# Optimization experiments

Measured on AMD Instinct MI355X. Metric: run time of the kernel, lower is better.

Reference implementation:

```python
import jax, jax.numpy as jnp
import numpy as np

B, S, D = 2, 2048, 512
H, HD = 8, 64  # num_heads, hidden_dim; H*HD == D
FF = 2048
EPS = 1e-5


def layer_norm(x, gamma, beta):
    mu = jnp.mean(x, axis=-1, keepdims=True)
    var = jnp.mean(jnp.square(x - mu), axis=-1, keepdims=True)
    return (x - mu) * jax.lax.rsqrt(var + EPS) * gamma + beta


def setup_inputs() -> dict:
    key = jax.random.key(0)
    ks = jax.random.split(key, 16)
    s = 0.02
    return {
        "Q": jax.random.normal(ks[0], (B, S, D), jnp.float32),
        "K": jax.random.normal(ks[1], (B, S, D), jnp.float32),
        "V": jax.random.normal(ks[2], (B, S, D), jnp.float32),
        "mask": jax.random.randint(ks[3], (B, S, S), 0, 2, jnp.int32),
        "Wq": jax.random.normal(ks[4], (D, H * HD), jnp.float32) * s,
        "Wk": jax.random.normal(ks[5], (D, H * HD), jnp.float32) * s,
        "Wv": jax.random.normal(ks[6], (D, H * HD), jnp.float32) * s,
        "Wo": jax.random.normal(ks[7], (H * HD, D), jnp.float32) * s,
        "bo": jnp.zeros((D,), jnp.float32),
        "gamma": jnp.ones((D,), jnp.float32),
        "beta": jnp.zeros((D,), jnp.float32),
        "W1": jax.random.normal(ks[8], (D, FF), jnp.float32) * s,
        "b1": jnp.zeros((FF,), jnp.float32),
        "W2": jax.random.normal(ks[9], (FF, D), jnp.float32) * s,
        "b2": jnp.zeros((D,), jnp.float32),
    }


def reference(Q, K, V, mask, Wq, Wk, Wv, Wo, bo, gamma, beta, W1, b1, W2, b2):
    # NOTE: original torch code calls Z.masked_fill(...) non-inplace and drops
    # the result, so `mask` has no effect on the math. Sequence=False.
    X = V
    # Faithful (interleaving) reshape: [B, S, H*HD] -> [B*H, S, HD]
    q = (Q @ Wq).reshape(B * H, -1, HD)
    k = (K @ Wk).reshape(B * H, -1, HD)
    v = (V @ Wv).reshape(B * H, -1, HD)
    scale = jnp.sqrt(jnp.float32(D))  # sqrt(input_size[2]), not sqrt(hidden_dim)
    scores = jnp.einsum('bqd,bkd->bqk', q, k) / scale  # [B*H, S, S]
    attn = jax.nn.softmax(scores, axis=2)
    Z = jnp.einsum('bqk,bkd->bqd', attn, v)            # [B*H, S, HD]
    Z = Z.reshape(B, -1, H * HD) @ Wo + bo             # [B, S, D]
    Z = layer_norm(X + Z, gamma, beta)
    ffn = (Z @ W1 + b1) @ W2 + b2                      # no activation in source
    return layer_norm(Z + ffn, gamma, beta)
```

## Files before the change

### kernel.cpp

```cpp
#include <hip/hip_runtime.h>
#include <hip/hip_bf16.h>


typedef __hip_bfloat16 bf16;
typedef short s16x8 __attribute__((ext_vector_type(8)));
typedef short s16x4 __attribute__((ext_vector_type(4)));
typedef float f32x4 __attribute__((ext_vector_type(4)));

#if __has_builtin(__builtin_amdgcn_exp2f)
#define EXP2F(x) __builtin_amdgcn_exp2f(x)
#else
#define EXP2F(x) exp2f(x)
#endif

__device__ __forceinline__ int dtypeF32(const void* gamma) {
    return *(const unsigned int*)gamma == 0x3F800000u;
}
__device__ __forceinline__ float inElem(const void* p, size_t i, int f32) {
    return f32 ? ((const float*)p)[i]
               : __bfloat162float(((const bf16*)p)[i]);
}
__device__ __forceinline__ void outElem(void* p, size_t i, float v, int f32) {
    if (f32) ((float*)p)[i] = v;
    else     ((bf16*)p)[i] = __float2bfloat16(v);
}
__device__ __forceinline__ s16x8 load8bf(const void* p, size_t i, int f32) {
    if (f32) {
        const float* s = (const float*)p + i;
        const float4 a = *(const float4*)s;
        const float4 b = *(const float4*)(s + 4);
        bf16 t[8] = {__float2bfloat16(a.x), __float2bfloat16(a.y),
                     __float2bfloat16(a.z), __float2bfloat16(a.w),
                     __float2bfloat16(b.x), __float2bfloat16(b.y),
                     __float2bfloat16(b.z), __float2bfloat16(b.w)};
        return *(const s16x8*)t;
    }
    return *(const s16x8*)((const bf16*)p + i);
}

__global__ __launch_bounds__(256) void tr_kernel(const void* __restrict__ s0,
                                                 const void* __restrict__ s1,
                                                 const void* __restrict__ s2,
                                                 const void* __restrict__ s3,
                                                 const void* __restrict__ s4,
                                                 bf16* __restrict__ WT4,
                                                 bf16* __restrict__ W2T,
                                                 float scale0,
                                                 const void* __restrict__ gamma) {
    const int z = blockIdx.z;
    if (z < 4 && blockIdx.y >= 16) return;
    const int f32 = dtypeF32(gamma);
    const void* src = z == 0 ? s0 : (z == 1 ? s1 : (z == 2 ? s2 : (z == 3 ? s3 : s4)));
    const int R = (z == 4) ? 2048 : 512;
    const int C = 512;
    bf16* d = (z == 4) ? W2T : WT4 + (size_t)z * 512 * 512;
    const float sc = (z == 0) ? scale0 : 1.f;
    __shared__ bf16 T[32][33];
    const int tx = threadIdx.x & 31, ty = threadIdx.x >> 5;
    const int c0 = blockIdx.x * 32, r0 = blockIdx.y * 32;
#pragma unroll
    for (int i = 0; i < 4; ++i)
        T[ty + 8 * i][tx] = __float2bfloat16(
            sc * inElem(src, (size_t)(r0 + ty + 8 * i) * C + c0 + tx, f32));
    __syncthreads();
#pragma unroll
    for (int i = 0; i < 4; ++i)
        d[(size_t)(c0 + ty + 8 * i) * R + r0 + tx] = T[tx][ty + 8 * i];
}

__global__ __launch_bounds__(64) void bc_kernel(const bf16* __restrict__ W2T,
                                                const void* __restrict__ b1,
                                                const void* __restrict__ b2,
                                                const void* __restrict__ bo,
                                                float* __restrict__ bc,
                                                float* __restrict__ bo_f,
                                                const void* __restrict__ gamma) {
    const int f32 = dtypeF32(gamma);
    const int n = blockIdx.x, lane = threadIdx.x;
    const bf16* row = W2T + (size_t)n * 2048;
    float s = 0.f;
#pragma unroll
    for (int i = 0; i < 32; ++i) {
        const int f = lane + 64 * i;
        s += inElem(b1, f, f32) * __bfloat162float(row[f]);
    }
#pragma unroll
    for (int off = 32; off; off >>= 1) s += __shfl_xor(s, off);
    if (lane == 0) {
        bc[n] = s + inElem(b2, n, f32);
        bo_f[n] = inElem(bo, n, f32);
    }
}

__global__ __launch_bounds__(256) void gemm_ks_kernel(
    const bf16* __restrict__ A, const void* __restrict__ Bt,
    float* __restrict__ Cf, const void* __restrict__ gamma) {
    __shared__ __align__(16) unsigned short As[64][40];
    __shared__ __align__(16) unsigned short Bs[128][40];

    const int bF = dtypeF32(gamma);
    const int N = 512, K = 2048, kSlice = 512;
    const int tid = threadIdx.x;
    const int w = tid >> 6, lane = tid & 63, quad = lane >> 4, l16 = lane & 15;
    const int wr = w >> 1, wc = w & 1;
    const int row0 = blockIdx.y * 64, col0 = blockIdx.x * 128;
    const int sr = tid >> 2, sc = (tid & 3) * 8;
    const int kOff = blockIdx.z * kSlice;
    float* C = Cf + (size_t)blockIdx.z * N * N;

    f32x4 acc[2][4];
#pragma unroll
    for (int rb = 0; rb < 2; ++rb)
#pragma unroll
        for (int nb = 0; nb < 4; ++nb) acc[rb][nb] = (f32x4){0.f, 0.f, 0.f, 0.f};

    for (int k0 = kOff; k0 < kOff + kSlice; k0 += 32) {
        __syncthreads();
        *(s16x8*)&As[sr][sc] = *(const s16x8*)(A + (size_t)(row0 + sr) * K + k0 + sc);
        *(s16x8*)&Bs[sr][sc] = load8bf(Bt, (size_t)(col0 + sr) * K + k0 + sc, bF);
        *(s16x8*)&Bs[sr + 64][sc] = load8bf(Bt, (size_t)(col0 + sr + 64) * K + k0 + sc, bF);
        __syncthreads();

        s16x8 aF[2], bFr[4];
#pragma unroll
        for (int rb = 0; rb < 2; ++rb)
            aF[rb] = *(const s16x8*)&As[wr * 32 + rb * 16 + l16][quad * 8];
#pragma unroll
        for (int nb = 0; nb < 4; ++nb)
            bFr[nb] = *(const s16x8*)&Bs[wc * 64 + nb * 16 + l16][quad * 8];
#pragma unroll
        for (int rb = 0; rb < 2; ++rb)
#pragma unroll
            for (int nb = 0; nb < 4; ++nb)
                acc[rb][nb] = __builtin_amdgcn_mfma_f32_16x16x32_bf16(
                    aF[rb], bFr[nb], acc[rb][nb], 0, 0, 0);
    }

#pragma unroll
    for (int rb = 0; rb < 2; ++rb)
#pragma unroll
        for (int nb = 0; nb < 4; ++nb) {
            const int col = col0 + wc * 64 + nb * 16 + l16;
#pragma unroll
            for (int r = 0; r < 4; ++r) {
                const int row = row0 + wr * 32 + rb * 16 + quad * 4 + r;
                C[(size_t)row * N + col] = acc[rb][nb][r];
            }
        }
}

__global__ __launch_bounds__(256) void combine4_kernel(const float* __restrict__ Cf,
                                                       bf16* __restrict__ WcT) {
    const int i0 = (blockIdx.x * 256 + threadIdx.x) * 4;
    const int MN = 512 * 512;
#pragma unroll
    for (int j = 0; j < 4; ++j) {
        const int i = i0 + j;
        WcT[i] = __float2bfloat16(Cf[i] + Cf[i + MN] + Cf[i + 2 * MN] + Cf[i + 3 * MN]);
    }
}

__global__ __launch_bounds__(256) void gemm_qkv_kernel(
    const void* __restrict__ Q, const void* __restrict__ K,
    const void* __restrict__ V,
    const bf16* __restrict__ WT4, bf16* __restrict__ Cbase,
    const void* __restrict__ gamma) {
    __shared__ __align__(16) unsigned short As[64][40];
    __shared__ __align__(16) unsigned short Bs[256][40];

    const int aF = dtypeF32(gamma);
    const int z = blockIdx.z;
    const void* A = z == 0 ? Q : (z == 1 ? K : V);
    const bf16* Bt = WT4 + (size_t)z * 512 * 512;
    bf16* C = Cbase + (size_t)z * 4096 * 512;

    const int tid = threadIdx.x;
    const int w = tid >> 6, lane = tid & 63, quad = lane >> 4, l16 = lane & 15;
    const int wr = w >> 1, wc = w & 1;
    const int row0 = blockIdx.y * 64, col0 = blockIdx.x * 256;
    const int sr = tid >> 2, sc = (tid & 3) * 8;

    f32x4 acc[2][8];
#pragma unroll
    for (int rb = 0; rb < 2; ++rb)
#pragma unroll
        for (int nb = 0; nb < 8; ++nb) acc[rb][nb] = (f32x4){0.f, 0.f, 0.f, 0.f};

    for (int k0 = 0; k0 < 512; k0 += 32) {
        __syncthreads();
        *(s16x8*)&As[sr][sc] = load8bf(A, (size_t)(row0 + sr) * 512 + k0 + sc, aF);
#pragma unroll
        for (int i = 0; i < 4; ++i) {
            const int br = sr + 64 * i;
            *(s16x8*)&Bs[br][sc] = *(const s16x8*)(Bt + (size_t)(col0 + br) * 512 + k0 + sc);
        }
        __syncthreads();

        s16x8 aFr[2];
#pragma unroll
        for (int rb = 0; rb < 2; ++rb)
            aFr[rb] = *(const s16x8*)&As[wr * 32 + rb * 16 + l16][quad * 8];
#pragma unroll
        for (int nb = 0; nb < 8; ++nb) {
            const s16x8 bFr = *(const s16x8*)&Bs[wc * 128 + nb * 16 + l16][quad * 8];
#pragma unroll
            for (int rb = 0; rb < 2; ++rb)
                acc[rb][nb] = __builtin_amdgcn_mfma_f32_16x16x32_bf16(
                    aFr[rb], bFr, acc[rb][nb], 0, 0, 0);
        }
    }

#pragma unroll
    for (int rb = 0; rb < 2; ++rb)
#pragma unroll
        for (int nb = 0; nb < 8; ++nb) {
            const int col = col0 + wc * 128 + nb * 16 + l16;
#pragma unroll
            for (int r = 0; r < 4; ++r) {
                const int row = row0 + wr * 32 + rb * 16 + quad * 4 + r;
                C[(size_t)row * 512 + col] = __float2bfloat16(acc[rb][nb][r]);
            }
        }
}

__global__ __launch_bounds__(256) void pack_kernel(const bf16* __restrict__ Kp,
                                                   const bf16* __restrict__ Vp,
                                                   bf16* __restrict__ KF,
                                                   bf16* __restrict__ VF) {
    const int b = blockIdx.x;
    if (b < 1024) {
        const int fid = b * 256 + threadIdx.x;
        const int lane = fid & 63, l16 = lane & 15, quad = lane >> 4;
        const int ks = (fid >> 6) & 1;
        const int jb = (fid >> 7) & 127;
        const int g = fid >> 14;
        const bf16* src = Kp + ((size_t)g * 2048 + jb * 16 + l16) * 64 + ks * 32 + quad * 8;
        *(s16x8*)(KF + (size_t)fid * 8) = *(const s16x8*)src;
    } else {
        const int fid = (b - 1024) * 256 + threadIdx.x;
        const int lane = fid & 63, l16 = lane & 15, quad = lane >> 4;
        const int db = (fid >> 6) & 3;
        const int jb = (fid >> 8) & 127;
        const int g = fid >> 15;
        bf16 t[4];
#pragma unroll
        for (int r = 0; r < 4; ++r)
            t[r] = Vp[((size_t)g * 2048 + jb * 16 + quad * 4 + r) * 64 + db * 16 + l16];
        *(s16x4*)(VF + (size_t)fid * 4) = *(const s16x4*)t;
    }
}

__global__ __launch_bounds__(256) void attn_mfma_kernel(const bf16* __restrict__ Qp,
                                                        const bf16* __restrict__ KF,
                                                        const bf16* __restrict__ VF,
                                                        bf16* __restrict__ Z) {
    const int SG = 2048;
    __shared__ __align__(16) unsigned short KsF[2][4096];
    __shared__ __align__(16) unsigned short VsF[2][4096];

    const int tid = threadIdx.x;
    const int w = tid >> 6;
    const int lane = tid & 63;
    const int quad = lane >> 4;
    const int l16 = lane & 15;

    const int g = blockIdx.x & 15;
    const int qt = blockIdx.x >> 4;
    const int qrow = g * SG + qt * 64 + w * 16 + l16;

    s16x8 bQ[2];
#pragma unroll
    for (int ks = 0; ks < 2; ++ks)
        bQ[ks] = *(const s16x8*)(Qp + (size_t)qrow * 64 + ks * 32 + quad * 8);

    f32x4 o[4];
#pragma unroll
    for (int db = 0; db < 4; ++db) o[db] = (f32x4){0.f, 0.f, 0.f, 0.f};
    f32x4 oSum = (f32x4){0.f, 0.f, 0.f, 0.f};
    const s16x4 aOnes = {(short)0x3F80, (short)0x3F80, (short)0x3F80, (short)0x3F80};

    const bf16* KFg = KF + (size_t)g * 131072;
    const bf16* VFg = VF + (size_t)g * 131072;

    s16x8 pk[2], pv[2];
#pragma unroll
    for (int i = 0; i < 2; ++i) {
        const int idx = tid + 256 * i;
        pk[i] = *(const s16x8*)(KFg + (size_t)idx * 8);
        pv[i] = *(const s16x8*)(VFg + (size_t)idx * 8);
    }
#pragma unroll
    for (int i = 0; i < 2; ++i) {
        const int idx = tid + 256 * i;
        *(s16x8*)&KsF[0][idx * 8] = pk[i];
        *(s16x8*)&VsF[0][idx * 8] = pv[i];
    }
    __syncthreads();

    for (int t = 0; t < 32; ++t) {
        const int cur = t & 1, nxt = cur ^ 1;
        if (t + 1 < 32) {
            const bf16* kt = KFg + (size_t)(t + 1) * 4096;
            const bf16* vt = VFg + (size_t)(t + 1) * 4096;
#pragma unroll
            for (int i = 0; i < 2; ++i) {
                const int idx = tid + 256 * i;
                pk[i] = *(const s16x8*)(kt + (size_t)idx * 8);
                pv[i] = *(const s16x8*)(vt + (size_t)idx * 8);
            }
        }

        f32x4 st[4];
#pragma unroll
        for (int kb = 0; kb < 4; ++kb) st[kb] = (f32x4){0.f, 0.f, 0.f, 0.f};
#pragma unroll
        for (int kb = 0; kb < 4; ++kb)
#pragma unroll
            for (int ks = 0; ks < 2; ++ks) {
                const s16x8 aK = *(const s16x8*)&KsF[cur][((kb * 2 + ks) * 64 + lane) * 8];
                st[kb] = __builtin_amdgcn_mfma_f32_16x16x32_bf16(aK, bQ[ks], st[kb], 0, 0, 0);
            }

        s16x4 bP[4];
#pragma unroll
        for (int kb = 0; kb < 4; ++kb) {
            const float p0 = EXP2F(st[kb][0]);
            const float p1 = EXP2F(st[kb][1]);
            const float p2 = EXP2F(st[kb][2]);
            const float p3 = EXP2F(st[kb][3]);
            const unsigned lo = __builtin_amdgcn_perm(
                __builtin_bit_cast(unsigned, p1), __builtin_bit_cast(unsigned, p0), 0x07060302u);
            const unsigned hi = __builtin_amdgcn_perm(
                __builtin_bit_cast(unsigned, p3), __builtin_bit_cast(unsigned, p2), 0x07060302u);
            union { unsigned u[2]; s16x4 v; } cvt;
            cvt.u[0] = lo; cvt.u[1] = hi;
            bP[kb] = cvt.v;
        }

#pragma unroll
        for (int kb = 0; kb < 4; ++kb) {
            oSum = __builtin_amdgcn_mfma_f32_16x16x16bf16_1k(aOnes, bP[kb], oSum, 0, 0, 0);
#pragma unroll
            for (int db = 0; db < 4; ++db) {
                const s16x4 aV = *(const s16x4*)&VsF[cur][((kb * 4 + db) * 64 + lane) * 4];
                o[db] = __builtin_amdgcn_mfma_f32_16x16x16bf16_1k(aV, bP[kb], o[db], 0, 0, 0);
            }
        }

        if (t + 1 < 32) {
            __syncthreads();
#pragma unroll
            for (int i = 0; i < 2; ++i) {
                const int idx = tid + 256 * i;
                *(s16x8*)&KsF[nxt][idx * 8] = pk[i];
                *(s16x8*)&VsF[nxt][idx * 8] = pv[i];
            }
            __syncthreads();
        }
    }

    const float inv = 1.f / oSum[0];
#pragma unroll
    for (int db = 0; db < 4; ++db) {
        bf16 tmp[4];
#pragma unroll
        for (int r = 0; r < 4; ++r) tmp[r] = __float2bfloat16(o[db][r] * inv);
        *(s16x4*)(Z + (size_t)qrow * 64 + db * 16 + quad * 4) = *(const s16x4*)tmp;
    }
}

__global__ __launch_bounds__(256) void gemm_bt_kernel(
    const bf16* __restrict__ A, const bf16* __restrict__ Bt,
    const float* __restrict__ bias, bf16* __restrict__ C,
    int M, int N, int K) {
    __shared__ __align__(16) unsigned short As[64][40];
    __shared__ __align__(16) unsigned short Bs[128][40];

    const int tid = threadIdx.x;
    const int w = tid >> 6, lane = tid & 63, quad = lane >> 4, l16 = lane & 15;
    const int wr = w >> 1, wc = w & 1;
    const int row0 = blockIdx.y * 64, col0 = blockIdx.x * 128;
    const int sr = tid >> 2, sc = (tid & 3) * 8;

    f32x4 acc[2][4];
#pragma unroll
    for (int rb = 0; rb < 2; ++rb)
#pragma unroll
        for (int nb = 0; nb < 4; ++nb) acc[rb][nb] = (f32x4){0.f, 0.f, 0.f, 0.f};

    for (int k0 = 0; k0 < K; k0 += 32) {
        __syncthreads();
        *(s16x8*)&As[sr][sc] = *(const s16x8*)(A + (size_t)(row0 + sr) * K + k0 + sc);
        *(s16x8*)&Bs[sr][sc] = *(const s16x8*)(Bt + (size_t)(col0 + sr) * K + k0 + sc);
        *(s16x8*)&Bs[sr + 64][sc] = *(const s16x8*)(Bt + (size_t)(col0 + sr + 64) * K + k0 + sc);
        __syncthreads();

        s16x8 aF[2], bF[4];
#pragma unroll
        for (int rb = 0; rb < 2; ++rb)
            aF[rb] = *(const s16x8*)&As[wr * 32 + rb * 16 + l16][quad * 8];
#pragma unroll
        for (int nb = 0; nb < 4; ++nb)
            bF[nb] = *(const s16x8*)&Bs[wc * 64 + nb * 16 + l16][quad * 8];
#pragma unroll
        for (int rb = 0; rb < 2; ++rb)
#pragma unroll
            for (int nb = 0; nb < 4; ++nb)
                acc[rb][nb] = __builtin_amdgcn_mfma_f32_16x16x32_bf16(
                    aF[rb], bF[nb], acc[rb][nb], 0, 0, 0);
    }

#pragma unroll
    for (int rb = 0; rb < 2; ++rb)
#pragma unroll
        for (int nb = 0; nb < 4; ++nb) {
            const int col = col0 + wc * 64 + nb * 16 + l16;
            const float bv = bias[col];
#pragma unroll
            for (int r = 0; r < 4; ++r) {
                const int row = row0 + wr * 32 + rb * 16 + quad * 4 + r;
                C[(size_t)row * N + col] = __float2bfloat16(acc[rb][nb][r] + bv);
            }
        }
}

__global__ __launch_bounds__(256) void ln_res_kernel(const void* __restrict__ X, int xMode,
                                                     const bf16* __restrict__ Zin,
                                                     const void* __restrict__ gamma,
                                                     const void* __restrict__ beta,
                                                     void* __restrict__ out, int oMode) {
    const int f = dtypeF32(gamma);
    const int xF = xMode == 2 ? f : xMode;
    const int oF = oMode == 2 ? f : oMode;
    const int row = blockIdx.x * 4 + (threadIdx.x >> 6);
    const int lane = threadIdx.x & 63;
    const size_t rb = (size_t)row * 512;

    float v[8];
    float sum = 0.f, sumsq = 0.f;
#pragma unroll
    for (int i = 0; i < 8; ++i) {
        const int c = lane + 64 * i;
        const float x = inElem(X, rb + c, xF) + __bfloat162float(Zin[rb + c]);
        v[i] = x;
        sum += x;
        sumsq += x * x;
    }
#pragma unroll
    for (int off = 32; off; off >>= 1) {
        sum += __shfl_xor(sum, off);
        sumsq += __shfl_xor(sumsq, off);
    }
    const float mu = sum * (1.f / 512.f);
    const float var = sumsq * (1.f / 512.f) - mu * mu;
    const float rs = rsqrtf(var + 1e-5f);
#pragma unroll
    for (int i = 0; i < 8; ++i) {
        const int c = lane + 64 * i;
        const float gm = inElem(gamma, c, f);
        const float bt = inElem(beta, c, f);
        outElem(out, rb + c, (v[i] - mu) * rs * gm + bt, oF);
    }
}

extern "C" void kernel_launch(void* const* d_in, const int* in_sizes, int n_in,
                              void* d_out, int out_size, void* d_ws, size_t ws_size,
                              hipStream_t stream) {
    const void* Q     = d_in[0];
    const void* K     = d_in[1];
    const void* V     = d_in[2];
    const void* Wq    = d_in[4];
    const void* Wk    = d_in[5];
    const void* Wv    = d_in[6];
    const void* Wo    = d_in[7];
    const void* bo    = d_in[8];
    const void* gamma = d_in[9];
    const void* beta  = d_in[10];
    const void* W1    = d_in[11];
    const void* b1    = d_in[12];
    const void* W2    = d_in[13];
    const void* b2    = d_in[14];

    const int M = 4096;
    const size_t NT  = (size_t)M * 512;
    const size_t WSQ = 512 * 512;
    const size_t W1N = 512 * 2048;

    const size_t NEED = 27000000;
    char* scratch = (ws_size >= NEED) ? (char*)d_ws : (char*)d_in[3];

    bf16* base = (bf16*)scratch;
    bf16* Qp  = base;
    bf16* Kp  = Qp + NT;
    bf16* Vp  = Kp + NT;
    bf16* KF  = Vp + NT;
    bf16* VF  = KF + NT;
    bf16* WT4 = VF + NT;
    bf16* W2T = WT4 + 4 * WSQ;
    bf16* WcT = W2T + W1N;
    float* bc   = (float*)(WcT + WSQ);
    float* bo_f = bc + 512;
    float* Wc32 = (float*)VF;
    bf16* Zt = Kp;
    bf16* Zo = Qp;
    bf16* Z1 = Vp;
    bf16* Fo = KF;

    const dim3 blk(256);
    const float qscale = 1.4426950408889634f * 0.044194173824159216f;

    tr_kernel<<<dim3(16, 64, 5), blk, 0, stream>>>(Wq, Wk, Wv, Wo, W2,
                                                   WT4, W2T, qscale, gamma);
    bc_kernel<<<dim3(512), dim3(64), 0, stream>>>(W2T, b1, b2, bo, bc, bo_f, gamma);

    gemm_ks_kernel<<<dim3(4, 8, 4), blk, 0, stream>>>(W2T, W1, Wc32, gamma);
    combine4_kernel<<<dim3(256), blk, 0, stream>>>(Wc32, WcT);

    gemm_qkv_kernel<<<dim3(2, 64, 3), blk, 0, stream>>>(Q, K, V, WT4, Qp, gamma);

    pack_kernel<<<dim3(3072), blk, 0, stream>>>(Kp, Vp, KF, VF);

    attn_mfma_kernel<<<dim3(512), blk, 0, stream>>>(Qp, KF, VF, Zt);

    gemm_bt_kernel<<<dim3(4, 64), blk, 0, stream>>>(Zt, WT4 + 3 * WSQ, bo_f,
                                                    Zo, M, 512, 512);
    ln_res_kernel<<<dim3(1024), blk, 0, stream>>>(V, 2, Zo, gamma, beta, Z1, 0);

    gemm_bt_kernel<<<dim3(4, 64), blk, 0, stream>>>(Z1, WcT, bc, Fo, M, 512, 512);
    ln_res_kernel<<<dim3(1024), blk, 0, stream>>>(Z1, 0, Fo, gamma, beta, d_out, 2);
}
```

Baseline: 237.8 us.

## Use direct global-to-LDS loads and larger KV tiles in attention kernel

The attention kernel now copies K/V tiles from global memory straight into LDS with global_load_lds, so the data no longer passes through registers. It also doubles the tile to 128 keys, halving the loop trips and leaving one barrier per iteration instead of two. The intent is to cut register pressure, barrier overhead and load latency. The cost is twice the LDS (64KB per block), which may lower occupancy. Correctness also depends on global_load_lds completing before the single barrier without an explicit vmcnt wait.

```diff
diff --git a/kernel.cpp b/kernel.cpp
--- a/kernel.cpp
+++ b/kernel.cpp
@@ -36,6 +36,13 @@
         return *(const s16x8*)t;
     }
     return *(const s16x8*)((const bf16*)p + i);
+}
+
+__device__ __forceinline__ void gll16(const bf16* g, unsigned short* l) {
+    __builtin_amdgcn_global_load_lds(
+        (const __attribute__((address_space(1))) unsigned int*)(const void*)g,
+        (__attribute__((address_space(3))) unsigned int*)(void*)l,
+        16, 0, 0);
 }
 
 __global__ __launch_bounds__(256) void tr_kernel(const void* __restrict__ s0,
@@ -255,8 +262,8 @@
                                                         const bf16* __restrict__ VF,
                                                         bf16* __restrict__ Z) {
     const int SG = 2048;
-    __shared__ __align__(16) unsigned short KsF[2][4096];
-    __shared__ __align__(16) unsigned short VsF[2][4096];
+    __shared__ __align__(16) unsigned short KsF[2][8192];
+    __shared__ __align__(16) unsigned short VsF[2][8192];
 
     const int tid = threadIdx.x;
     const int w = tid >> 6;
@@ -282,81 +289,71 @@
     const bf16* KFg = KF + (size_t)g * 131072;
     const bf16* VFg = VF + (size_t)g * 131072;
 
-    s16x8 pk[2], pv[2];
-#pragma unroll
-    for (int i = 0; i < 2; ++i) {
-        const int idx = tid + 256 * i;
-        pk[i] = *(const s16x8*)(KFg + (size_t)idx * 8);
-        pv[i] = *(const s16x8*)(VFg + (size_t)idx * 8);
-    }
-#pragma unroll
-    for (int i = 0; i < 2; ++i) {
-        const int idx = tid + 256 * i;
-        *(s16x8*)&KsF[0][idx * 8] = pk[i];
-        *(s16x8*)&VsF[0][idx * 8] = pv[i];
+#pragma unroll
+    for (int c = 0; c < 4; ++c) {
+        const int idx = c * 256 + tid;
+        gll16(KFg + (size_t)idx * 8, &KsF[0][idx * 8]);
+        gll16(VFg + (size_t)idx * 8, &VsF[0][idx * 8]);
     }
     __syncthreads();
 
-    for (int t = 0; t < 32; ++t) {
+    for (int t = 0; t < 16; ++t) {
         const int cur = t & 1, nxt = cur ^ 1;
-        if (t + 1 < 32) {
-            const bf16* kt = KFg + (size_t)(t + 1) * 4096;
-            const bf16* vt = VFg + (size_t)(t + 1) * 4096;
-#pragma unroll
-            for (int i = 0; i < 2; ++i) {
-                const int idx = tid + 256 * i;
-                pk[i] = *(const s16x8*)(kt + (size_t)idx * 8);
-                pv[i] = *(const s16x8*)(vt + (size_t)idx * 8);
+        if (t < 15) {
+            const bf16* kt = KFg + (size_t)(t + 1) * 8192;
+            const bf16* vt = VFg + (size_t)(t + 1) * 8192;
+#pragma unroll
+            for (int c = 0; c < 4; ++c) {
+                const int idx = c * 256 + tid;
+                gll16(kt + (size_t)idx * 8, &KsF[nxt][idx * 8]);
+                gll16(vt + (size_t)idx * 8, &VsF[nxt][idx * 8]);
             }
         }
 
-        f32x4 st[4];
-#pragma unroll
-        for (int kb = 0; kb < 4; ++kb) st[kb] = (f32x4){0.f, 0.f, 0.f, 0.f};
-#pragma unroll
-        for (int kb = 0; kb < 4; ++kb)
-#pragma unroll
-            for (int ks = 0; ks < 2; ++ks) {
-                const s16x8 aK = *(const s16x8*)&KsF[cur][((kb * 2 + ks) * 64 + lane) * 8];
-                st[kb] = __builtin_amdgcn_mfma_f32_16x16x32_bf16(aK, bQ[ks], st[kb], 0, 0, 0);
+#pragma unroll
+        for (int h = 0; h < 2; ++h) {
+            const unsigned short* Kh = &KsF[cur][h * 4096];
+            const unsigned short* Vh = &VsF[cur][h * 4096];
+
+            f32x4 st[4];
+#pragma unroll
+            for (int kb = 0; kb < 4; ++kb) st[kb] = (f32x4){0.f, 0.f, 0.f, 0.f};
+#pragma unroll
+            for (int kb = 0; kb < 4; ++kb)
+#pragma unroll
+                for (int ks = 0; ks < 2; ++ks) {
+                    const s16x8 aK = *(const s16x8*)&Kh[((kb * 2 + ks) * 64 + lane) * 8];
+                    st[kb] = __builtin_amdgcn_mfma_f32_16x16x32_bf16(aK, bQ[ks], st[kb], 0, 0, 0);
+                }
+
+            s16x4 bP[4];
+#pragma unroll
+            for (int kb = 0; kb < 4; ++kb) {
+                const float p0 = EXP2F(st[kb][0]);
+                const float p1 = EXP2F(st[kb][1]);
+                const float p2 = EXP2F(st[kb][2]);
+                const float p3 = EXP2F(st[kb][3]);
+                const unsigned lo = __builtin_amdgcn_perm(
+                    __builtin_bit_cast(unsigned, p1), __builtin_bit_cast(unsigned, p0), 0x07060302u);
+                const unsigned hi = __builtin_amdgcn_perm(
+                    __builtin_bit_cast(unsigned, p3), __builtin_bit_cast(unsigned, p2), 0x07060302u);
+                union { unsigned u[2]; s16x4 v; } cvt;
+                cvt.u[0] = lo; cvt.u[1] = hi;
+                bP[kb] = cvt.v;
             }
 
-        s16x4 bP[4];
-#pragma unroll
-        for (int kb = 0; kb < 4; ++kb) {
-            const float p0 = EXP2F(st[kb][0]);
-            const float p1 = EXP2F(st[kb][1]);
-            const float p2 = EXP2F(st[kb][2]);
-            const float p3 = EXP2F(st[kb][3]);
-            const unsigned lo = __builtin_amdgcn_perm(
-                __builtin_bit_cast(unsigned, p1), __builtin_bit_cast(unsigned, p0), 0x07060302u);
-            const unsigned hi = __builtin_amdgcn_perm(
-                __builtin_bit_cast(unsigned, p3), __builtin_bit_cast(unsigned, p2), 0x07060302u);
-            union { unsigned u[2]; s16x4 v; } cvt;
-            cvt.u[0] = lo; cvt.u[1] = hi;
-            bP[kb] = cvt.v;
-        }
-
-#pragma unroll
-        for (int kb = 0; kb < 4; ++kb) {
-            oSum = __builtin_amdgcn_mfma_f32_16x16x16bf16_1k(aOnes, bP[kb], oSum, 0, 0, 0);
-#pragma unroll
-            for (int db = 0; db < 4; ++db) {
-                const s16x4 aV = *(const s16x4*)&VsF[cur][((kb * 4 + db) * 64 + lane) * 4];
-                o[db] = __builtin_amdgcn_mfma_f32_16x16x16bf16_1k(aV, bP[kb], o[db], 0, 0, 0);
+#pragma unroll
+            for (int kb = 0; kb < 4; ++kb) {
+                oSum = __builtin_amdgcn_mfma_f32_16x16x16bf16_1k(aOnes, bP[kb], oSum, 0, 0, 0);
+#pragma unroll
+                for (int db = 0; db < 4; ++db) {
+                    const s16x4 aV = *(const s16x4*)&Vh[((kb * 4 + db) * 64 + lane) * 4];
+                    o[db] = __builtin_amdgcn_mfma_f32_16x16x16bf16_1k(aV, bP[kb], o[db], 0, 0, 0);
+                }
             }
         }
 
-        if (t + 1 < 32) {
-            __syncthreads();
-#pragma unroll
-            for (int i = 0; i < 2; ++i) {
-                const int idx = tid + 256 * i;
-                *(s16x8*)&KsF[nxt][idx * 8] = pk[i];
-                *(s16x8*)&VsF[nxt][idx * 8] = pv[i];
-            }
-            __syncthreads();
-        }
+        if (t < 15) __syncthreads();
     }
 
     const float inv = 1.f / oSum[0];
```

Result: no change. 237.1 us (-0.3%).
